# Optimization experiments

Measured on AMD Instinct MI355X. Metric: run time of the kernel, lower is better.

The kernel has to match this reference:

```python
import jax, jax.numpy as jnp
import numpy as np

N_NODES = 50000
N_EDGES = 800000
NF = 128
HC = 128
NC = 40


def sage_conv(x, src, dst, Wl, Wr, b, num_nodes):
    """PyG SAGEConv with mean aggregation:
    out = lin_l(mean_{j in N(i)} x_j) + lin_r(x_i), bias folded into lin_l."""
    msgs = x[src]                                             # [E, F] gather
    agg = jax.ops.segment_sum(msgs, dst, num_segments=num_nodes)  # [N, F]
    cnt = jax.ops.segment_sum(jnp.ones((src.shape[0],), dtype=x.dtype), dst,
                              num_segments=num_nodes)          # [N]
    mean = agg / jnp.clip(cnt, 1.0)[:, None]                   # mean aggregation
    return mean @ Wl.T + x @ Wr.T + b


def setup_inputs() -> dict:
    key = jax.random.key(0)
    k = jax.random.split(key, 8)
    x = jax.random.normal(k[0], (N_NODES, NF), dtype=jnp.float32)
    edge_index = jax.random.randint(k[1], (2, N_EDGES), 0, N_NODES, dtype=jnp.int32)
    s1 = 1.0 / np.sqrt(NF)
    s2 = 1.0 / np.sqrt(HC)
    Wl1 = jax.random.uniform(k[2], (HC, NF), jnp.float32, -s1, s1)
    Wr1 = jax.random.uniform(k[3], (HC, NF), jnp.float32, -s1, s1)
    b1 = jnp.zeros((HC,), jnp.float32)
    Wl2 = jax.random.uniform(k[4], (NC, HC), jnp.float32, -s2, s2)
    Wr2 = jax.random.uniform(k[5], (NC, HC), jnp.float32, -s2, s2)
    b2 = jnp.zeros((NC,), jnp.float32)
    return {"x": x, "edge_index": edge_index, "Wl1": Wl1, "Wr1": Wr1,
            "b1": b1, "Wl2": Wl2, "Wr2": Wr2, "b2": b2}


def reference(x, edge_index, Wl1, Wr1, b1, Wl2, Wr2, b2):
    src, dst = edge_index[0], edge_index[1]
    num_nodes = x.shape[0]
    emb = sage_conv(x, src, dst, Wl1, Wr1, b1, num_nodes)      # embedding_output
    h = jax.nn.relu(emb)
    # F.dropout with training=False is the identity (inference reference)
    logits = sage_conv(h, src, dst, Wl2, Wr2, b2, num_nodes)
    return (logits, emb)
```

## Files before the change

### kernel.cpp

```cpp
#include <hip/hip_runtime.h>
#include <hip/hip_bf16.h>
#include <stdint.h>

#define NODES 50000
#define EDGES 800000
#define CAP   64

typedef __attribute__((ext_vector_type(8))) short bf16x8;
typedef __attribute__((ext_vector_type(8))) unsigned short u16x8;
typedef __attribute__((ext_vector_type(4))) float f32x4;
typedef unsigned short ushort_t;

__device__ __forceinline__ float4 ld4(const float* p) {
    return *reinterpret_cast<const float4*>(p);
}
__device__ __forceinline__ ushort_t f2bf(float f) {
    unsigned u = __float_as_uint(f);
    unsigned r = (u + 0x7fff + ((u >> 16) & 1)) >> 16;
    return (ushort_t)r;
}
__device__ __forceinline__ float bf2f(ushort_t h) {
    return __uint_as_float(((unsigned)h) << 16);
}

__global__ __launch_bounds__(256) void prep(
    const float* __restrict__ x, const int* __restrict__ src,
    const int* __restrict__ dst,
    const float* __restrict__ Wr1, const float* __restrict__ Wl1,
    const float* __restrict__ Wr2, const float* __restrict__ Wl2,
    int* __restrict__ deg, ushort_t* __restrict__ esrc,
    ushort_t* __restrict__ A1, ushort_t* __restrict__ w1p,
    ushort_t* __restrict__ w2p) {
    int b = blockIdx.x;
    if (b < 3128) {
        int g = b & 7, chunk = b >> 3;
        int lo = g * 6250;
#pragma unroll
        for (int k = 0; k < 8; ++k) {
            int e = chunk * 2048 + k * 256 + threadIdx.x;
            if (e < EDGES) {
                int d = dst[e];
                if ((unsigned)(d - lo) < 6250u) {
                    int s = src[e];
                    int p = atomicAdd(&deg[d], 1);
                    if (p < CAP) esrc[(size_t)d * CAP + p] = (ushort_t)s;
                }
            }
        }
    } else if (b < 9378) {
        int idx = (b - 3128) * 256 + threadIdx.x;
        int i = idx >> 5, c = idx & 31;
        float4 v = ld4(x + (size_t)i * 128 + c * 4);
        ushort4 h;
        h.x = f2bf(v.x); h.y = f2bf(v.y); h.z = f2bf(v.z); h.w = f2bf(v.w);
        *reinterpret_cast<ushort4*>(A1 + (size_t)i * 256 + c * 4) = h;
    } else if (b < 9394) {
        int t = (b - 9378) * 256 + threadIdx.x;
        int nf = t >> 9, kc = (t >> 6) & 7, lane = t & 63;
        int r = nf * 16 + (lane & 15);
        int k2 = kc * 32 + ((lane >> 4) << 3);
        u16x8 o;
#pragma unroll
        for (int j = 0; j < 8; ++j) {
            int kk = k2 + j;
            float v = (kk < 128) ? Wr1[r * 128 + kk] : Wl1[r * 128 + (kk - 128)];
            o[j] = f2bf(v);
        }
        *reinterpret_cast<u16x8*>(w1p + (size_t)t * 8) = o;
    } else {
        int t = (b - 9394) * 256 + threadIdx.x;
        if (t >= 1280) return;
        int nf = t >> 8, kc = (t >> 6) & 3, lane = t & 63;
        int r = nf * 16 + (lane & 15);
        int k2 = kc * 32 + ((lane >> 4) << 3);
        u16x8 o;
#pragma unroll
        for (int j = 0; j < 8; ++j) {
            int kk = k2 + j;
            float v = (r < 40) ? Wr2[r * 128 + kk] : Wl2[(r - 40) * 128 + kk];
            o[j] = f2bf(v);
        }
        *reinterpret_cast<u16x8*>(w2p + (size_t)t * 8) = o;
    }
}

__global__ __launch_bounds__(256) void aggx(
    ushort_t* __restrict__ A1, const ushort_t* __restrict__ esrc,
    const int* __restrict__ deg) {
    int idx = blockIdx.x * 256 + threadIdx.x;
    int i = idx >> 4, c = idx & 15;
    if (i >= NODES) return;
    int dg = deg[i];
    int n = dg < CAP ? dg : CAP;
    const ushort_t* ep = esrc + (size_t)i * CAP;
    float a0[8] = {}, a1[8] = {};
    int j = 0;
    for (; j + 4 <= n; j += 4) {
        int s0 = ep[j], s1 = ep[j + 1], s2 = ep[j + 2], s3 = ep[j + 3];
        u16x8 v0 = *reinterpret_cast<const u16x8*>(A1 + (size_t)s0 * 256 + c * 8);
        u16x8 v1 = *reinterpret_cast<const u16x8*>(A1 + (size_t)s1 * 256 + c * 8);
        u16x8 v2 = *reinterpret_cast<const u16x8*>(A1 + (size_t)s2 * 256 + c * 8);
        u16x8 v3 = *reinterpret_cast<const u16x8*>(A1 + (size_t)s3 * 256 + c * 8);
#pragma unroll
        for (int k = 0; k < 8; ++k) {
            a0[k] += bf2f(v0[k]) + bf2f(v2[k]);
            a1[k] += bf2f(v1[k]) + bf2f(v3[k]);
        }
    }
    for (; j < n; ++j) {
        int s = ep[j];
        u16x8 v = *reinterpret_cast<const u16x8*>(A1 + (size_t)s * 256 + c * 8);
#pragma unroll
        for (int k = 0; k < 8; ++k) a0[k] += bf2f(v[k]);
    }
    float ci = 1.0f / fmaxf((float)dg, 1.0f);
    u16x8 m;
#pragma unroll
    for (int k = 0; k < 8; ++k) m[k] = f2bf((a0[k] + a1[k]) * ci);
    *reinterpret_cast<u16x8*>(A1 + (size_t)i * 256 + 128 + c * 8) = m;
}

__global__ __launch_bounds__(256) void gemm12(
    const ushort_t* __restrict__ A1, const ushort_t* __restrict__ w1p,
    const ushort_t* __restrict__ w2p, const float* __restrict__ b1,
    float* __restrict__ emb, ushort_t* __restrict__ V, int M) {
    __shared__ ushort_t hs[64][136];
    const int wave = threadIdx.x >> 6, lane = threadIdx.x & 63;
    const int r0 = blockIdx.x * 64 + wave * 16;
    int arow = r0 + (lane & 15); if (arow >= M) arow = M - 1;
    const int klane = (lane >> 4) * 8;

    f32x4 acc[8] = {};
#pragma unroll
    for (int kc = 0; kc < 8; ++kc) {
        bf16x8 a = *reinterpret_cast<const bf16x8*>(A1 + (size_t)arow * 256 + kc * 32 + klane);
        bf16x8 wv[8];
#pragma unroll
        for (int nf = 0; nf < 8; ++nf)
            wv[nf] = *reinterpret_cast<const bf16x8*>(
                w1p + (size_t)((nf * 8 + kc) * 64 + lane) * 8);
#pragma unroll
        for (int nf = 0; nf < 8; ++nf)
            acc[nf] = __builtin_amdgcn_mfma_f32_16x16x32_bf16(a, wv[nf], acc[nf], 0, 0, 0);
    }

    const int crow0r = wave * 16 + (lane >> 4) * 4;
    const int crow0  = blockIdx.x * 64 + crow0r;
    const int ccol   = lane & 15;
#pragma unroll
    for (int nf = 0; nf < 8; ++nf) {
        int col = nf * 16 + ccol;
        float bv = b1[col];
#pragma unroll
        for (int r = 0; r < 4; ++r) {
            int row = crow0 + r;
            float val = acc[nf][r] + bv;
            if (row < M) emb[(size_t)row * 128 + col] = val;
            hs[crow0r + r][col] = f2bf(fmaxf(val, 0.f));
        }
    }
    __syncthreads();

    f32x4 acc2[5] = {};
#pragma unroll
    for (int kc = 0; kc < 4; ++kc) {
        bf16x8 a = *reinterpret_cast<const bf16x8*>(
            &hs[wave * 16 + (lane & 15)][kc * 32 + klane]);
        bf16x8 wv[5];
#pragma unroll
        for (int nf = 0; nf < 5; ++nf)
            wv[nf] = *reinterpret_cast<const bf16x8*>(
                w2p + (size_t)((nf * 4 + kc) * 64 + lane) * 8);
#pragma unroll
        for (int nf = 0; nf < 5; ++nf)
            acc2[nf] = __builtin_amdgcn_mfma_f32_16x16x32_bf16(a, wv[nf], acc2[nf], 0, 0, 0);
    }
#pragma unroll
    for (int nf = 0; nf < 5; ++nf) {
        int col = nf * 16 + ccol;
#pragma unroll
        for (int r = 0; r < 4; ++r) {
            int row = crow0 + r;
            if (row < M) V[(size_t)row * 80 + col] = f2bf(acc2[nf][r]);
        }
    }
}

__global__ __launch_bounds__(256) void agg2(
    const ushort_t* __restrict__ V, const ushort_t* __restrict__ esrc,
    const int* __restrict__ deg, const float* __restrict__ b2,
    float* __restrict__ logits) {
    int idx = blockIdx.x * 256 + threadIdx.x;
    int i = idx >> 3, c = idx & 7;
    if (i >= NODES || c >= 5) return;
    int dg = deg[i];
    int n = dg < CAP ? dg : CAP;
    const ushort_t* ep = esrc + (size_t)i * CAP;
    float a0[8] = {}, a1[8] = {};
    int j = 0;
    for (; j + 4 <= n; j += 4) {
        int s0 = ep[j], s1 = ep[j + 1], s2 = ep[j + 2], s3 = ep[j + 3];
        u16x8 v0 = *reinterpret_cast<const u16x8*>(V + (size_t)s0 * 80 + 40 + c * 8);
        u16x8 v1 = *reinterpret_cast<const u16x8*>(V + (size_t)s1 * 80 + 40 + c * 8);
        u16x8 v2 = *reinterpret_cast<const u16x8*>(V + (size_t)s2 * 80 + 40 + c * 8);
        u16x8 v3 = *reinterpret_cast<const u16x8*>(V + (size_t)s3 * 80 + 40 + c * 8);
#pragma unroll
        for (int k = 0; k < 8; ++k) {
            a0[k] += bf2f(v0[k]) + bf2f(v2[k]);
            a1[k] += bf2f(v1[k]) + bf2f(v3[k]);
        }
    }
    for (; j < n; ++j) {
        int s = ep[j];
        u16x8 v = *reinterpret_cast<const u16x8*>(V + (size_t)s * 80 + 40 + c * 8);
#pragma unroll
        for (int k = 0; k < 8; ++k) a0[k] += bf2f(v[k]);
    }
    float ci = 1.0f / fmaxf((float)dg, 1.0f);
    u16x8 sv = *reinterpret_cast<const u16x8*>(V + (size_t)i * 80 + c * 8);
    float o[8];
#pragma unroll
    for (int k = 0; k < 8; ++k)
        o[k] = bf2f(sv[k]) + (a0[k] + a1[k]) * ci + b2[c * 8 + k];
    float4* dst4 = reinterpret_cast<float4*>(logits + (size_t)i * 40 + c * 8);
    dst4[0] = make_float4(o[0], o[1], o[2], o[3]);
    dst4[1] = make_float4(o[4], o[5], o[6], o[7]);
}

extern "C" void kernel_launch(void* const* d_in, const int* in_sizes, int n_in,
                              void* d_out, int out_size, void* d_ws, size_t ws_size,
                              hipStream_t stream) {
    const float* x   = (const float*)d_in[0];
    const int*   ei  = (const int*)d_in[1];
    const float* Wl1 = (const float*)d_in[2];
    const float* Wr1 = (const float*)d_in[3];
    const float* b1  = (const float*)d_in[4];
    const float* Wl2 = (const float*)d_in[5];
    const float* Wr2 = (const float*)d_in[6];
    const float* b2  = (const float*)d_in[7];
    const int* src = ei;
    const int* dst = ei + EDGES;

    char* ws = (char*)d_ws;
    ushort_t* A1   = (ushort_t*)ws;
    ushort_t* V    = (ushort_t*)(ws + 25600000);
    ushort_t* esrc = (ushort_t*)(ws + 33600000);
    int*      deg  = (int*)(ws + 40000000);
    ushort_t* w1p  = (ushort_t*)(ws + 40200000);
    ushort_t* w2p  = (ushort_t*)(ws + 40265536);

    float* logits_out = (float*)d_out;
    float* emb_out    = logits_out + (size_t)NODES * 40;

    hipMemsetAsync(deg, 0, (size_t)NODES * 4, stream);

    prep<<<9399, 256, 0, stream>>>(x, src, dst, Wr1, Wl1, Wr2, Wl2,
                                   deg, esrc, A1, w1p, w2p);

    aggx<<<3125, 256, 0, stream>>>(A1, esrc, deg);

    gemm12<<<(NODES + 63) / 64, 256, 0, stream>>>(A1, w1p, w2p, b1, emb_out, V, NODES);

    agg2<<<(NODES * 8 + 255) / 256, 256, 0, stream>>>(V, esrc, deg, b2, logits_out);
}
```

Before: 121.2 us.

## Unroll gathers by 8, nontemporal emb stores, replace memset with zero kernel

Both neighbor-aggregation kernels gain an 8-wide unrolled gather loop so more independent loads are in flight per thread. The fp32 embedding output is now written with nontemporal stores to keep it from polluting cache. The hipMemsetAsync on the degree array is replaced by a small custom zeroing kernel to cut launch overhead. The bounds check in aggx is dropped, which relies on the grid exactly covering NODES*16 threads; that holds for the current launch of 3125 blocks.

Measured after the change: 119.4 us, median of 2. Within noise of the previous version (-1.5%).

```diff
diff --git a/kernel.cpp b/kernel.cpp
--- a/kernel.cpp
+++ b/kernel.cpp
@@ -21,6 +21,11 @@
 }
 __device__ __forceinline__ float bf2f(ushort_t h) {
     return __uint_as_float(((unsigned)h) << 16);
+}
+
+__global__ __launch_bounds__(256) void zerok(int* __restrict__ deg) {
+    int t = blockIdx.x * 256 + threadIdx.x;
+    if (t < 25000) reinterpret_cast<int2*>(deg)[t] = make_int2(0, 0);
 }
 
 __global__ __launch_bounds__(256) void prep(
@@ -89,12 +94,28 @@
     const int* __restrict__ deg) {
     int idx = blockIdx.x * 256 + threadIdx.x;
     int i = idx >> 4, c = idx & 15;
-    if (i >= NODES) return;
     int dg = deg[i];
     int n = dg < CAP ? dg : CAP;
     const ushort_t* ep = esrc + (size_t)i * CAP;
     float a0[8] = {}, a1[8] = {};
     int j = 0;
+    for (; j + 8 <= n; j += 8) {
+        int s0 = ep[j],     s1 = ep[j + 1], s2 = ep[j + 2], s3 = ep[j + 3];
+        int s4 = ep[j + 4], s5 = ep[j + 5], s6 = ep[j + 6], s7 = ep[j + 7];
+        u16x8 v0 = *reinterpret_cast<const u16x8*>(A1 + (size_t)s0 * 256 + c * 8);
+        u16x8 v1 = *reinterpret_cast<const u16x8*>(A1 + (size_t)s1 * 256 + c * 8);
+        u16x8 v2 = *reinterpret_cast<const u16x8*>(A1 + (size_t)s2 * 256 + c * 8);
+        u16x8 v3 = *reinterpret_cast<const u16x8*>(A1 + (size_t)s3 * 256 + c * 8);
+        u16x8 v4 = *reinterpret_cast<const u16x8*>(A1 + (size_t)s4 * 256 + c * 8);
+        u16x8 v5 = *reinterpret_cast<const u16x8*>(A1 + (size_t)s5 * 256 + c * 8);
+        u16x8 v6 = *reinterpret_cast<const u16x8*>(A1 + (size_t)s6 * 256 + c * 8);
+        u16x8 v7 = *reinterpret_cast<const u16x8*>(A1 + (size_t)s7 * 256 + c * 8);
+#pragma unroll
+        for (int k = 0; k < 8; ++k) {
+            a0[k] += (bf2f(v0[k]) + bf2f(v2[k])) + (bf2f(v4[k]) + bf2f(v6[k]));
+            a1[k] += (bf2f(v1[k]) + bf2f(v3[k])) + (bf2f(v5[k]) + bf2f(v7[k]));
+        }
+    }
     for (; j + 4 <= n; j += 4) {
         int s0 = ep[j], s1 = ep[j + 1], s2 = ep[j + 2], s3 = ep[j + 3];
         u16x8 v0 = *reinterpret_cast<const u16x8*>(A1 + (size_t)s0 * 256 + c * 8);
@@ -155,7 +176,8 @@
         for (int r = 0; r < 4; ++r) {
             int row = crow0 + r;
             float val = acc[nf][r] + bv;
-            if (row < M) emb[(size_t)row * 128 + col] = val;
+            if (row < M)
+                __builtin_nontemporal_store(val, emb + (size_t)row * 128 + col);
             hs[crow0r + r][col] = f2bf(fmaxf(val, 0.f));
         }
     }
@@ -198,6 +220,23 @@
     const ushort_t* ep = esrc + (size_t)i * CAP;
     float a0[8] = {}, a1[8] = {};
     int j = 0;
+    for (; j + 8 <= n; j += 8) {
+        int s0 = ep[j],     s1 = ep[j + 1], s2 = ep[j + 2], s3 = ep[j + 3];
+        int s4 = ep[j + 4], s5 = ep[j + 5], s6 = ep[j + 6], s7 = ep[j + 7];
+        u16x8 v0 = *reinterpret_cast<const u16x8*>(V + (size_t)s0 * 80 + 40 + c * 8);
+        u16x8 v1 = *reinterpret_cast<const u16x8*>(V + (size_t)s1 * 80 + 40 + c * 8);
+        u16x8 v2 = *reinterpret_cast<const u16x8*>(V + (size_t)s2 * 80 + 40 + c * 8);
+        u16x8 v3 = *reinterpret_cast<const u16x8*>(V + (size_t)s3 * 80 + 40 + c * 8);
+        u16x8 v4 = *reinterpret_cast<const u16x8*>(V + (size_t)s4 * 80 + 40 + c * 8);
+        u16x8 v5 = *reinterpret_cast<const u16x8*>(V + (size_t)s5 * 80 + 40 + c * 8);
+        u16x8 v6 = *reinterpret_cast<const u16x8*>(V + (size_t)s6 * 80 + 40 + c * 8);
+        u16x8 v7 = *reinterpret_cast<const u16x8*>(V + (size_t)s7 * 80 + 40 + c * 8);
+#pragma unroll
+        for (int k = 0; k < 8; ++k) {
+            a0[k] += (bf2f(v0[k]) + bf2f(v2[k])) + (bf2f(v4[k]) + bf2f(v6[k]));
+            a1[k] += (bf2f(v1[k]) + bf2f(v3[k])) + (bf2f(v5[k]) + bf2f(v7[k]));
+        }
+    }
     for (; j + 4 <= n; j += 4) {
         int s0 = ep[j], s1 = ep[j + 1], s2 = ep[j + 2], s3 = ep[j + 3];
         u16x8 v0 = *reinterpret_cast<const u16x8*>(V + (size_t)s0 * 80 + 40 + c * 8);
@@ -252,7 +291,7 @@
     float* logits_out = (float*)d_out;
     float* emb_out    = logits_out + (size_t)NODES * 40;
 
-    hipMemsetAsync(deg, 0, (size_t)NODES * 4, stream);
+    zerok<<<98, 256, 0, stream>>>(deg);
 
     prep<<<9399, 256, 0, stream>>>(x, src, dst, Wr1, Wl1, Wr2, Wl2,
                                    deg, esrc, A1, w1p, w2p);
```
